# Kernel tuning notes

Measured on AMD Instinct MI355X. Metric: run time of the kernel, lower is better.

The kernel has to match this reference:

```python
import jax, jax.numpy as jnp
import numpy as np

# Static config (from set_param of the wrapped deformable conv)
N, CIN, H, W = 8, 64, 128, 128
COUT, KH, KW = 64, 3, 3
STRIDE, PAD, DIL = 1, 1, 1
WEIGHT_BIT = 8
K = KH * KW
HO = (H + 2 * PAD - DIL * (KH - 1) - 1) // STRIDE + 1
WO = (W + 2 * PAD - DIL * (KW - 1) - 1) // STRIDE + 1


def setup_inputs() -> dict:
    key = jax.random.key(0)
    k1, k2, k3 = jax.random.split(key, 3)
    x = jax.random.normal(k1, (N, CIN, H, W), dtype=jnp.float32)
    offset = jax.random.normal(k2, (N, 2 * K, HO, WO), dtype=jnp.float32)
    weight = jax.random.normal(k3, (COUT, CIN, KH, KW), dtype=jnp.float32) * 0.05
    return {"x": x, "offset": offset, "weight": weight}


def quantize_weight_symmetric(w, bits):
    # HAWQ/CoDeNet symmetric per-tensor quant: scale = max(|min|,|max|)/n,
    # q = clamp(round(w/scale), -n-1, n) * scale, straight-through estimator.
    n = 2 ** (bits - 1) - 1
    sat = jnp.maximum(jnp.abs(w.min()), jnp.abs(w.max()))
    scale = jnp.maximum(sat, 1e-8) / n
    wq = jnp.clip(jnp.round(w / scale), -n - 1, n) * scale
    return w + jax.lax.stop_gradient(wq - w)


def deform_conv2d(x, offset, weight):
    # x: [N,C,H,W]; offset: [N, 2*K, HO, WO] (y,x interleaved per kernel tap)
    # Base sampling grid for each kernel tap and output location.
    ky, kx = jnp.meshgrid(jnp.arange(KH), jnp.arange(KW), indexing='ij')
    ky = ky.reshape(K).astype(jnp.float32)  # [K]
    kx = kx.reshape(K).astype(jnp.float32)
    ho = jnp.arange(HO, dtype=jnp.float32)
    wo = jnp.arange(WO, dtype=jnp.float32)
    base_y = ho[None, :, None] * STRIDE - PAD + ky[:, None, None] * DIL  # [K,HO,1]
    base_x = wo[None, None, :] * STRIDE - PAD + kx[:, None, None] * DIL  # [K,1,WO]

    off = offset.reshape(N, K, 2, HO, WO)
    py = base_y[None] + off[:, :, 0]  # [N,K,HO,WO]
    px = base_x[None] + off[:, :, 1]

    y0 = jnp.floor(py)
    x0 = jnp.floor(px)
    dy = py - y0
    dx = px - x0
    y0i = y0.astype(jnp.int32)
    x0i = x0.astype(jnp.int32)

    xf = x.reshape(N, CIN, H * W)

    def gather_corner(yi, xi, wgt):
        # zero padding outside the image
        valid = (yi >= 0) & (yi < H) & (xi >= 0) & (xi < W)
        idx = jnp.clip(yi, 0, H - 1) * W + jnp.clip(xi, 0, W - 1)  # [N,K,HO,WO]
        vals = jax.vmap(lambda xn, idn: xn[:, idn.reshape(-1)])(xf, idx)
        vals = vals.reshape(N, CIN, K, HO, WO)
        return vals * (wgt * valid.astype(wgt.dtype))[:, None]  # [N,1,K,HO,WO]

    sampled = (
        gather_corner(y0i, x0i, (1.0 - dy) * (1.0 - dx))
        + gather_corner(y0i, x0i + 1, (1.0 - dy) * dx)
        + gather_corner(y0i + 1, x0i, dy * (1.0 - dx))
        + gather_corner(y0i + 1, x0i + 1, dy * dx)
    )  # [N,CIN,K,HO,WO]

    out = jnp.einsum('nckhw,ock->nohw', sampled, weight.reshape(COUT, CIN, K))
    return out


def reference(x, offset, weight):
    wq = quantize_weight_symmetric(weight, WEIGHT_BIT)
    return deform_conv2d(x, offset, wq)
```

## Files before the change

kernel.cpp:

```cpp
#include <hip/hip_runtime.h>
#include <hip/hip_bf16.h>

#define NB    8
#define CCH   64
#define HH    128
#define WW    128
#define KTAP  9
#define HW    (HH * WW)
#define KSTEPS 18
#define NW    36864

typedef _Float16 f16x8 __attribute__((ext_vector_type(8)));
typedef _Float16 f16x2 __attribute__((ext_vector_type(2)));
typedef __attribute__((ext_vector_type(4))) float f32x4;

__device__ inline unsigned int pack_f16(float a, float b) {
    f16x2 h;
    h[0] = (_Float16)a;
    h[1] = (_Float16)b;
    return __builtin_bit_cast(unsigned int, h);
}

__device__ inline f16x8 as_f16x8(uint4 u) { return __builtin_bit_cast(f16x8, u); }

__device__ inline void lds_barrier() {
    asm volatile("s_waitcnt lgkmcnt(0)\n\ts_barrier" ::: "memory");
}

__global__ __launch_bounds__(256) void prep_kernel(const float* __restrict__ x,
                                                   const float* __restrict__ w,
                                                   unsigned int* __restrict__ xt32,
                                                   uint4* __restrict__ bq) {
    __shared__ float tile[64 * 65];
    const int t = threadIdx.x;
    const int bid = blockIdx.x;

    if (bid < 2048) {
        const int n = bid >> 8;
        const int pbase = (bid & 255) * 64;
        #pragma unroll
        for (int i = 0; i < 4; i++) {
            int idx = i * 256 + t;
            int c = idx >> 4, f4 = idx & 15;
            float4 v = *(const float4*)&x[((size_t)(n * CCH + c)) * HW + pbase + f4 * 4];
            float* d = &tile[c * 65 + f4 * 4];
            d[0] = v.x; d[1] = v.y; d[2] = v.z; d[3] = v.w;
        }
        __syncthreads();
        const int px = t >> 2, c4 = t & 3;
        float f[16];
        #pragma unroll
        for (int j = 0; j < 16; j++) f[j] = tile[(c4 * 16 + j) * 65 + px];
        unsigned int o8[8];
        #pragma unroll
        for (int i = 0; i < 8; i++) o8[i] = pack_f16(f[2 * i], f[2 * i + 1]);
        uint4* dst = (uint4*)&xt32[((size_t)(n * HW + pbase + px)) * 32 + c4 * 8];
        dst[0] = make_uint4(o8[0], o8[1], o8[2], o8[3]);
        dst[1] = make_uint4(o8[4], o8[5], o8[6], o8[7]);
    } else {
        float m0 = 0.f, m1 = 0.f, m2 = 0.f, m3 = 0.f;
        for (int i = t; i < NW; i += 1024) {
            m0 = fmaxf(m0, fabsf(w[i]));
            m1 = fmaxf(m1, fabsf(w[i + 256]));
            m2 = fmaxf(m2, fabsf(w[i + 512]));
            m3 = fmaxf(m3, fabsf(w[i + 768]));
        }
        float m = fmaxf(fmaxf(m0, m1), fmaxf(m2, m3));
        #pragma unroll
        for (int off = 32; off > 0; off >>= 1)
            m = fmaxf(m, __shfl_down(m, off));
        if ((t & 63) == 0) tile[t >> 6] = m;
        __syncthreads();
        m = fmaxf(fmaxf(tile[0], tile[1]), fmaxf(tile[2], tile[3]));
        const float scale = fmaxf(m, 1e-8f) / 127.f;
        const float inv_scale = 1.f / scale;

        const int rec = (bid - 2048) * 256 + t;
        int nt  = rec / (KSTEPS * 64);
        int rem = rec - nt * (KSTEPS * 64);
        int s    = rem >> 6;
        int lane = rem & 63;
        int quad = lane >> 4, n16 = lane & 15;
        int o = nt * 16 + n16;
        unsigned int u[4];
        #pragma unroll
        for (int jj = 0; jj < 4; jj++) {
            float q[2];
            #pragma unroll
            for (int h = 0; h < 2; h++) {
                int k   = s * 32 + quad * 8 + 2 * jj + h;
                int c   = k & 63;
                int tap = k >> 6;
                float v  = w[(o * CCH + c) * KTAP + tap];
                float qq = rintf(v * inv_scale);
                q[h] = fminf(fmaxf(qq, -128.f), 127.f) * scale;
            }
            u[jj] = pack_f16(q[0], q[1]);
        }
        bq[rec] = make_uint4(u[0], u[1], u[2], u[3]);
    }
}

__global__ __launch_bounds__(256, 8) void deform_mfma(const unsigned short* __restrict__ xt,
                                                      const float* __restrict__ offset,
                                                      const uint4* __restrict__ bq,
                                                      float* __restrict__ out) {
    __shared__ __align__(16) _Float16 Abuf[4096];
    __shared__ unsigned int SC[576];
    __shared__ uint2 SW[576];

    const int t    = threadIdx.x;
    const int wid  = t >> 6;
    const int lane = t & 63;
    const int quad = lane >> 4, n16 = lane & 15;
    const int bid  = blockIdx.x;
    const int n    = bid & 7;
    const int px0  = (bid >> 3) * 64;
    const int pg   = t >> 3;
    const int q8   = t & 7;

    const char* xb = (const char*)(xt + (size_t)n * HW * CCH);
    const float* offn = offset + (size_t)n * 2 * KTAP * HW;

    for (int u = t; u < 576; u += 256) {
        const int tap = u >> 6, p = u & 63;
        const int ppx = px0 + p;
        const int ho = ppx >> 7, wo = ppx & 127;
        const int ky = tap / 3, kx = tap - 3 * ky;
        const float py  = (float)(ho - 1 + ky) + offn[(2 * tap) * HW + ppx];
        const float pxf = (float)(wo - 1 + kx) + offn[(2 * tap + 1) * HW + ppx];
        const float fy = floorf(py), fx = floorf(pxf);
        const int y0 = (int)fy, x0 = (int)fx;
        const float dy = py - fy, dx = pxf - fx;
        const int y1 = y0 + 1, x1 = x0 + 1;
        const bool vy0 = (y0 >= 0) && (y0 < HH);
        const bool vy1 = (y1 >= 0) && (y1 < HH);
        const bool vx0 = (x0 >= 0) && (x0 < WW);
        const bool vx1 = (x1 >= 0) && (x1 < WW);
        const int y0c = min(max(y0, 0), HH - 1);
        const int y1c = min(max(y1, 0), HH - 1);
        const int x0c = min(max(x0, 0), WW - 1);
        const int x1c = min(max(x1, 0), WW - 1);
        const float w00 = (1.f - dy) * (1.f - dx) * ((vy0 && vx0) ? 1.f : 0.f);
        const float w01 = (1.f - dy) * dx         * ((vy0 && vx1) ? 1.f : 0.f);
        const float w10 = dy * (1.f - dx)         * ((vy1 && vx0) ? 1.f : 0.f);
        const float w11 = dy * dx                 * ((vy1 && vx1) ? 1.f : 0.f);
        SC[u] = (unsigned)(y0c | (x0c << 7) | (y1c << 14) | (x1c << 21));
        SW[u] = make_uint2(pack_f16(w00, w01), pack_f16(w10, w11));
    }
    __syncthreads();

    f32x4 acc[4];
    #pragma unroll
    for (int mt = 0; mt < 4; mt++) acc[mt] = (f32x4){0.f, 0.f, 0.f, 0.f};

    uint4 bset[2][2];

    auto blend_stage = [&](int s) {
        #pragma unroll
        for (int rr = 0; rr < 2; rr++) {
            const int p = pg + 32 * rr;
            const unsigned int cc = SC[s * 64 + p];
            const uint2 wwp = SW[s * 64 + p];
            const int y0b = (int)(cc & 127) << 14;
            const int x0b = (int)((cc >> 7) & 127) << 7;
            const int y1b = (int)((cc >> 14) & 127) << 14;
            const int x1b = (int)(cc >> 21) << 7;
            const char* base = xb + q8 * 16;
            const uint4 c00 = *(const uint4*)(base + (y0b | x0b));
            const uint4 c01 = *(const uint4*)(base + (y0b | x1b));
            const uint4 c10 = *(const uint4*)(base + (y1b | x0b));
            const uint4 c11 = *(const uint4*)(base + (y1b | x1b));
            const f16x2 wA = __builtin_bit_cast(f16x2, wwp.x);
            const f16x2 wB = __builtin_bit_cast(f16x2, wwp.y);
            f16x8 sa = as_f16x8(c00) * wA[0];
            sa += as_f16x8(c01) * wA[1];
            sa += as_f16x8(c10) * wB[0];
            sa += as_f16x8(c11) * wB[1];
            *(f16x8*)&Abuf[p * 64 + ((q8 ^ (p & 7)) * 8)] = sa;
        }
    };
    auto mma_stage = [&](int s) {
        #pragma unroll
        for (int ks = 0; ks < 2; ks++) {
            const f16x8 bf = __builtin_bit_cast(f16x8, bset[s & 1][ks]);
            const int slot = (ks * 4 + quad) ^ (n16 & 7);
            #pragma unroll
            for (int mt = 0; mt < 4; mt++) {
                const int rr = mt * 16 + n16;
                const f16x8 a = *(const f16x8*)&Abuf[rr * 64 + slot * 8];
                acc[mt] = __builtin_amdgcn_mfma_f32_16x16x32_f16(a, bf, acc[mt], 0, 0, 0);
            }
        }
    };

    bset[0][0] = bq[((size_t)wid * KSTEPS + 0) * 64 + lane];
    bset[0][1] = bq[((size_t)wid * KSTEPS + 1) * 64 + lane];

    #pragma unroll
    for (int s = 0; s < 9; s++) {
        blend_stage(s);
        if (s < 8) {
            bset[(s + 1) & 1][0] = bq[((size_t)wid * KSTEPS + 2 * (s + 1)) * 64 + lane];
            bset[(s + 1) & 1][1] = bq[((size_t)wid * KSTEPS + 2 * (s + 1) + 1) * 64 + lane];
        }
        lds_barrier();
        mma_stage(s);
        lds_barrier();
    }

    const int o = wid * 16 + n16;
    #pragma unroll
    for (int mt = 0; mt < 4; mt++) {
        float4 v = make_float4(acc[mt].x, acc[mt].y, acc[mt].z, acc[mt].w);
        float* dst = out + ((size_t)(n * CCH + o)) * HW + px0 + mt * 16 + quad * 4;
        *(float4*)dst = v;
    }
}

extern "C" void kernel_launch(void* const* d_in, const int* in_sizes, int n_in,
                              void* d_out, int out_size, void* d_ws, size_t ws_size,
                              hipStream_t stream) {
    const float* x      = (const float*)d_in[0];
    const float* offset = (const float*)d_in[1];
    const float* weight = (const float*)d_in[2];
    float* out = (float*)d_out;

    unsigned char* ws = (unsigned char*)d_ws;
    uint4*        bq   = (uint4*)ws;
    unsigned int* xt32 = (unsigned int*)(ws + 131072);
    const unsigned short* xt = (const unsigned short*)xt32;

    prep_kernel<<<2048 + 18, 256, 0, stream>>>(x, weight, xt32, bq);
    deform_mfma<<<2048, 256, 0, stream>>>(xt, offset, bq, out);
}
```

Baseline: 132.1 us.

## Give each wave its own pixel slice to drop block barriers in MFMA loop

After: 144.5 us. 1.09x slower.

```diff
diff --git a/kernel.cpp b/kernel.cpp
--- a/kernel.cpp
+++ b/kernel.cpp
@@ -23,10 +23,6 @@
 
 __device__ inline f16x8 as_f16x8(uint4 u) { return __builtin_bit_cast(f16x8, u); }
 
-__device__ inline void lds_barrier() {
-    asm volatile("s_waitcnt lgkmcnt(0)\n\ts_barrier" ::: "memory");
-}
-
 __global__ __launch_bounds__(256) void prep_kernel(const float* __restrict__ x,
                                                    const float* __restrict__ w,
                                                    unsigned int* __restrict__ xt32,
@@ -36,8 +32,8 @@
     const int bid = blockIdx.x;
 
     if (bid < 2048) {
-        const int n = bid >> 8;
-        const int pbase = (bid & 255) * 64;
+        const int n = bid & 7;
+        const int pbase = ((bid >> 3) & 255) * 64;
         #pragma unroll
         for (int i = 0; i < 4; i++) {
             int idx = i * 256 + t;
@@ -101,11 +97,11 @@
     }
 }
 
-__global__ __launch_bounds__(256, 8) void deform_mfma(const unsigned short* __restrict__ xt,
+__global__ __launch_bounds__(256, 6) void deform_mfma(const unsigned short* __restrict__ xt,
                                                       const float* __restrict__ offset,
                                                       const uint4* __restrict__ bq,
                                                       float* __restrict__ out) {
-    __shared__ __align__(16) _Float16 Abuf[4096];
+    __shared__ __align__(16) _Float16 Abuf[4][1024];
     __shared__ unsigned int SC[576];
     __shared__ uint2 SW[576];
 
@@ -113,11 +109,12 @@
     const int wid  = t >> 6;
     const int lane = t & 63;
     const int quad = lane >> 4, n16 = lane & 15;
+    const int p8   = lane >> 3;
+    const int q8   = lane & 7;
     const int bid  = blockIdx.x;
     const int n    = bid & 7;
     const int px0  = (bid >> 3) * 64;
-    const int pg   = t >> 3;
-    const int q8   = t & 7;
+    const int wpx0 = wid * 16;
 
     const char* xb = (const char*)(xt + (size_t)n * HW * CCH);
     const float* offn = offset + (size_t)n * 2 * KTAP * HW;
@@ -152,16 +149,23 @@
 
     f32x4 acc[4];
     #pragma unroll
-    for (int mt = 0; mt < 4; mt++) acc[mt] = (f32x4){0.f, 0.f, 0.f, 0.f};
-
-    uint4 bset[2][2];
-
-    auto blend_stage = [&](int s) {
-        #pragma unroll
-        for (int rr = 0; rr < 2; rr++) {
-            const int p = pg + 32 * rr;
-            const unsigned int cc = SC[s * 64 + p];
-            const uint2 wwp = SW[s * 64 + p];
+    for (int nt = 0; nt < 4; nt++) acc[nt] = (f32x4){0.f, 0.f, 0.f, 0.f};
+
+    _Float16* my = Abuf[wid];
+
+    for (int s = 0; s < 9; s++) {
+        uint4 bfr[8];
+        #pragma unroll
+        for (int ks = 0; ks < 2; ks++)
+            #pragma unroll
+            for (int nt = 0; nt < 4; nt++)
+                bfr[ks * 4 + nt] = bq[((size_t)nt * KSTEPS + 2 * s + ks) * 64 + lane];
+
+        #pragma unroll
+        for (int o = 0; o < 2; o++) {
+            const int pl = wpx0 + o * 8 + p8;
+            const unsigned int cc = SC[s * 64 + pl];
+            const uint2 wwp = SW[s * 64 + pl];
             const int y0b = (int)(cc & 127) << 14;
             const int x0b = (int)((cc >> 7) & 127) << 7;
             const int y1b = (int)((cc >> 14) & 127) << 14;
@@ -177,43 +181,27 @@
             sa += as_f16x8(c01) * wA[1];
             sa += as_f16x8(c10) * wB[0];
             sa += as_f16x8(c11) * wB[1];
-            *(f16x8*)&Abuf[p * 64 + ((q8 ^ (p & 7)) * 8)] = sa;
-        }
-    };
-    auto mma_stage = [&](int s) {
+            *(f16x8*)&my[(o * 8 + p8) * 64 + ((q8 ^ p8) * 8)] = sa;
+        }
+
         #pragma unroll
         for (int ks = 0; ks < 2; ks++) {
-            const f16x8 bf = __builtin_bit_cast(f16x8, bset[s & 1][ks]);
-            const int slot = (ks * 4 + quad) ^ (n16 & 7);
+            const int c8 = ks * 4 + quad;
+            const int slot = c8 ^ (n16 & 7);
+            const f16x8 a = *(const f16x8*)&my[n16 * 64 + slot * 8];
             #pragma unroll
-            for (int mt = 0; mt < 4; mt++) {
-                const int rr = mt * 16 + n16;
-                const f16x8 a = *(const f16x8*)&Abuf[rr * 64 + slot * 8];
-                acc[mt] = __builtin_amdgcn_mfma_f32_16x16x32_f16(a, bf, acc[mt], 0, 0, 0);
+            for (int nt = 0; nt < 4; nt++) {
+                const f16x8 bf = __builtin_bit_cast(f16x8, bfr[ks * 4 + nt]);
+                acc[nt] = __builtin_amdgcn_mfma_f32_16x16x32_f16(a, bf, acc[nt], 0, 0, 0);
             }
         }
-    };
-
-    bset[0][0] = bq[((size_t)wid * KSTEPS + 0) * 64 + lane];
-    bset[0][1] = bq[((size_t)wid * KSTEPS + 1) * 64 + lane];
+    }
 
     #pragma unroll
-    for (int s = 0; s < 9; s++) {
-        blend_stage(s);
-        if (s < 8) {
-            bset[(s + 1) & 1][0] = bq[((size_t)wid * KSTEPS + 2 * (s + 1)) * 64 + lane];
-            bset[(s + 1) & 1][1] = bq[((size_t)wid * KSTEPS + 2 * (s + 1) + 1) * 64 + lane];
-        }
-        lds_barrier();
-        mma_stage(s);
-        lds_barrier();
-    }
-
-    const int o = wid * 16 + n16;
-    #pragma unroll
-    for (int mt = 0; mt < 4; mt++) {
-        float4 v = make_float4(acc[mt].x, acc[mt].y, acc[mt].z, acc[mt].w);
-        float* dst = out + ((size_t)(n * CCH + o)) * HW + px0 + mt * 16 + quad * 4;
+    for (int nt = 0; nt < 4; nt++) {
+        const int oc = nt * 16 + n16;
+        float4 v = make_float4(acc[nt].x, acc[nt].y, acc[nt].z, acc[nt].w);
+        float* dst = out + ((size_t)(n * CCH + oc)) * HW + px0 + wpx0 + quad * 4;
         *(float4*)dst = v;
     }
 }
```
